# Performance work log

Measured on AMD Instinct MI355X. Metric: run time of the kernel, lower is better.

The kernel has to match this reference:

```python
import jax, jax.numpy as jnp
import numpy as np

B, T, D = 1, 2048, 2048
H, HD = 16, 128          # n_heads, head_dim
RD = 64                  # rotary_emb_dim
K = 4                    # short conv kernel size
EPS = 1e-5


def setup_inputs() -> dict:
    key = jax.random.key(0)
    ks = jax.random.split(key, 10)
    hidden_states = jax.random.normal(ks[0], (B, T, D), dtype=jnp.float32)
    # standard RoPE tables for the rotary sub-dimension
    inv_freq = 1.0 / (10000.0 ** (jnp.arange(0, RD, 2, dtype=jnp.float32) / RD))  # [RD/2]
    pos = jnp.arange(T, dtype=jnp.float32)
    freqs = pos[:, None] * inv_freq[None, :]          # [T, RD/2]
    emb = jnp.concatenate([freqs, freqs], axis=-1)    # [T, RD]
    cos = jnp.broadcast_to(jnp.cos(emb)[None], (B, T, RD))
    sin = jnp.broadcast_to(jnp.sin(emb)[None], (B, T, RD))
    s = 1.0 / np.sqrt(D)
    return {
        "hidden_states": hidden_states,
        "cos": cos, "sin": sin,
        "Wq": jax.random.normal(ks[1], (D, D), jnp.float32) * s,
        "Wk": jax.random.normal(ks[2], (D, D), jnp.float32) * s,
        "Wv": jax.random.normal(ks[3], (D, D), jnp.float32) * s,
        "Wo": jax.random.normal(ks[4], (D, D), jnp.float32) * s,
        "conv_q_w": jax.random.normal(ks[5], (D, K), jnp.float32) * 0.5,
        "conv_k_w": jax.random.normal(ks[6], (D, K), jnp.float32) * 0.5,
        "conv_v_w": jax.random.normal(ks[7], (D, K), jnp.float32) * 0.5,
        "q_norm_w": jnp.ones((HD,), jnp.float32),
        "k_norm_w": jnp.ones((HD,), jnp.float32),
    }


def _causal_conv_silu(x, w):
    # x: [B,T,D], w: [D,K]; depthwise causal conv (tap K-1 hits current pos) + SiLU
    xp = jnp.pad(x, ((0, 0), (K - 1, 0), (0, 0)))
    y = sum(xp[:, j:j + T, :] * w[None, None, :, j] for j in range(K))
    return jax.nn.silu(y)


def _rms_norm(x, w):
    # x: [..., HD]
    var = jnp.mean(x * x, axis=-1, keepdims=True)
    return x * jax.lax.rsqrt(var + EPS) * w


def _rotate_half(x):
    x1, x2 = x[..., : x.shape[-1] // 2], x[..., x.shape[-1] // 2:]
    return jnp.concatenate([-x2, x1], axis=-1)


def _apply_rope(x, cos, sin):
    # x: [B,H,T,HD]; cos/sin: [B,T,RD] -> unsqueeze head dim; partial rotary branch
    cos = cos[:, None, :, :]
    sin = sin[:, None, :, :]
    x_rot, x_pass = x[..., :RD], x[..., RD:]
    x_rot = x_rot * cos + _rotate_half(x_rot) * sin
    # faithful to source: negates rotated part when rotary_dim != head_dim
    return jnp.concatenate([-x_rot, x_pass], axis=-1)


def reference(hidden_states, cos, sin, Wq, Wk, Wv, Wo,
              conv_q_w, conv_k_w, conv_v_w, q_norm_w, k_norm_w):
    # projections (Linear with bias=False: y = x @ W^T)
    q = hidden_states @ Wq.T
    k = hidden_states @ Wk.T
    v = hidden_states @ Wv.T
    # short causal depthwise conv + SiLU
    q = _causal_conv_silu(q, conv_q_w)
    k = _causal_conv_silu(k, conv_k_w)
    v = _causal_conv_silu(v, conv_v_w)
    # split heads: [B,T,D] -> [B,T,H,HD]
    q = q.reshape(B, T, H, HD)
    k = k.reshape(B, T, H, HD)
    v = v.reshape(B, T, H, HD)
    # per-head RMSNorm, then [B,H,T,HD]
    q = _rms_norm(q, q_norm_w).transpose(0, 2, 1, 3)
    k = _rms_norm(k, k_norm_w).transpose(0, 2, 1, 3)
    v = v.transpose(0, 2, 1, 3)
    # RoPE (partial)
    q = _apply_rope(q, cos, sin)
    k = _apply_rope(k, cos, sin)
    # causal attention
    scale = 1.0 / np.sqrt(HD)
    scores = jnp.einsum('bhqd,bhkd->bhqk', q, k) * scale
    causal = jnp.tril(jnp.ones((T, T), dtype=bool))
    scores = jnp.where(causal[None, None], scores, jnp.float32(-1e30))
    probs = jax.nn.softmax(scores, axis=-1)
    attn = jnp.einsum('bhqk,bhkd->bhqd', probs, v)
    # [B,H,T,HD] -> [B,T,D], output projection
    out = attn.transpose(0, 2, 1, 3).reshape(B, T, D) @ Wo.T
    return out
```

## Files before the change

kernel.cpp:

```cpp
#include <hip/hip_runtime.h>
#include <hip/hip_bf16.h>

#define T_SEQ 2048
#define D_MODEL 2048
#define NH 16
#define HDIM 128
#define RD_ROT 64

typedef __bf16 bf16x8 __attribute__((ext_vector_type(8)));
typedef float f32x4 __attribute__((ext_vector_type(4)));

__device__ __forceinline__ void async_copy16(const __bf16* g, __bf16* l) {
    __builtin_amdgcn_global_load_lds(
        (const __attribute__((address_space(1))) void*)g,
        (__attribute__((address_space(3))) void*)l, 16, 0, 0);
}

__global__ __launch_bounds__(256) void cast_kernel(
    const float* __restrict__ s0, const float* __restrict__ s1, const float* __restrict__ s2,
    const float* __restrict__ s3, const float* __restrict__ s4,
    __bf16* __restrict__ d0, __bf16* __restrict__ d1, __bf16* __restrict__ d2,
    __bf16* __restrict__ d3, __bf16* __restrict__ d4)
{
    const float* s; __bf16* d;
    switch (blockIdx.y) {
        case 0: s = s0; d = d0; break;
        case 1: s = s1; d = d1; break;
        case 2: s = s2; d = d2; break;
        case 3: s = s3; d = d3; break;
        default: s = s4; d = d4; break;
    }
    size_t base = (size_t)blockIdx.x * D_MODEL + (size_t)threadIdx.x * 8;
    f32x4 a = *(const f32x4*)(s + base);
    f32x4 b = *(const f32x4*)(s + base + 4);
    bf16x8 o;
    #pragma unroll
    for (int i = 0; i < 4; i++) { o[i] = (__bf16)a[i]; o[i + 4] = (__bf16)b[i]; }
    *(bf16x8*)(d + base) = o;
}

__global__ __launch_bounds__(256) void gemm_bt_kernel(
    const __bf16* __restrict__ A,
    const __bf16* __restrict__ B0, const __bf16* __restrict__ B1, const __bf16* __restrict__ B2,
    __bf16* __restrict__ C0, __bf16* __restrict__ C1, __bf16* __restrict__ C2)
{
    constexpr int BM = 128, BK = 64, KD = D_MODEL;
    const __bf16* Bm = blockIdx.z == 0 ? B0 : (blockIdx.z == 1 ? B1 : B2);
    __bf16* Cm       = blockIdx.z == 0 ? C0 : (blockIdx.z == 1 ? C1 : C2);

    __shared__ __align__(16) __bf16 As[BM * BK];
    __shared__ __align__(16) __bf16 Bs[BM * BK];

    const int lane = threadIdx.x & 63;
    const int wave = threadIdx.x >> 6;
    const int r15  = lane & 15;
    const int quad = lane >> 4;
    const int bm = blockIdx.x * BM;
    const int bn = blockIdx.y * BM;
    const int wm = (wave >> 1) * 64;
    const int wn = (wave & 1) * 64;

    f32x4 acc[4][4] = {};

    const int srow_l = lane >> 3;
    const int sg     = lane & 7;

    for (int k0 = 0; k0 < KD; k0 += BK) {
        #pragma unroll
        for (int c = 0; c < 4; c++) {
            int row = wave * 32 + c * 8 + srow_l;
            int g = sg ^ (row & 7);
            async_copy16(A  + (size_t)(bm + row) * KD + k0 + g * 8, &As[(wave * 32 + c * 8) * BK]);
            async_copy16(Bm + (size_t)(bn + row) * KD + k0 + g * 8, &Bs[(wave * 32 + c * 8) * BK]);
        }
        __syncthreads();

        #pragma unroll
        for (int kc = 0; kc < 2; kc++) {
            bf16x8 av[4], bv[4];
            #pragma unroll
            for (int mt = 0; mt < 4; mt++)
                av[mt] = *(const bf16x8*)&As[(wm + mt * 16 + r15) * BK + (((kc * 4 + quad) ^ (r15 & 7)) << 3)];
            #pragma unroll
            for (int nt = 0; nt < 4; nt++)
                bv[nt] = *(const bf16x8*)&Bs[(wn + nt * 16 + r15) * BK + (((kc * 4 + quad) ^ (r15 & 7)) << 3)];
            #pragma unroll
            for (int mt = 0; mt < 4; mt++)
                #pragma unroll
                for (int nt = 0; nt < 4; nt++)
                    acc[mt][nt] = __builtin_amdgcn_mfma_f32_16x16x32_bf16(av[mt], bv[nt], acc[mt][nt], 0, 0, 0);
        }
        __syncthreads();
    }

    #pragma unroll
    for (int mt = 0; mt < 4; mt++) {
        #pragma unroll
        for (int r = 0; r < 4; r++) {
            size_t row = bm + wm + mt * 16 + quad * 4 + r;
            #pragma unroll
            for (int nt = 0; nt < 4; nt++) {
                size_t col = bn + wn + nt * 16 + r15;
                Cm[row * D_MODEL + col] = (__bf16)acc[mt][nt][r];
            }
        }
    }
}

__global__ __launch_bounds__(256) void gemm_bt_splitk_kernel(
    const __bf16* __restrict__ A, const __bf16* __restrict__ Bm, float* __restrict__ C)
{
    constexpr int BM = 128, BK = 64, KD = D_MODEL;
    __shared__ __align__(16) __bf16 As[BM * BK];
    __shared__ __align__(16) __bf16 Bs[BM * BK];

    const int lane = threadIdx.x & 63;
    const int wave = threadIdx.x >> 6;
    const int r15  = lane & 15;
    const int quad = lane >> 4;
    const int bm = blockIdx.x * BM;
    const int bn = blockIdx.y * BM;
    const int wm = (wave >> 1) * 64;
    const int wn = (wave & 1) * 64;
    const int kbase = blockIdx.z * (KD / 2);

    f32x4 acc[4][4] = {};
    const int srow_l = lane >> 3;
    const int sg     = lane & 7;

    for (int k0 = kbase; k0 < kbase + KD / 2; k0 += BK) {
        #pragma unroll
        for (int c = 0; c < 4; c++) {
            int row = wave * 32 + c * 8 + srow_l;
            int g = sg ^ (row & 7);
            async_copy16(A  + (size_t)(bm + row) * KD + k0 + g * 8, &As[(wave * 32 + c * 8) * BK]);
            async_copy16(Bm + (size_t)(bn + row) * KD + k0 + g * 8, &Bs[(wave * 32 + c * 8) * BK]);
        }
        __syncthreads();

        #pragma unroll
        for (int kc = 0; kc < 2; kc++) {
            bf16x8 av[4], bv[4];
            #pragma unroll
            for (int mt = 0; mt < 4; mt++)
                av[mt] = *(const bf16x8*)&As[(wm + mt * 16 + r15) * BK + (((kc * 4 + quad) ^ (r15 & 7)) << 3)];
            #pragma unroll
            for (int nt = 0; nt < 4; nt++)
                bv[nt] = *(const bf16x8*)&Bs[(wn + nt * 16 + r15) * BK + (((kc * 4 + quad) ^ (r15 & 7)) << 3)];
            #pragma unroll
            for (int mt = 0; mt < 4; mt++)
                #pragma unroll
                for (int nt = 0; nt < 4; nt++)
                    acc[mt][nt] = __builtin_amdgcn_mfma_f32_16x16x32_bf16(av[mt], bv[nt], acc[mt][nt], 0, 0, 0);
        }
        __syncthreads();
    }

    #pragma unroll
    for (int mt = 0; mt < 4; mt++) {
        #pragma unroll
        for (int r = 0; r < 4; r++) {
            size_t row = bm + wm + mt * 16 + quad * 4 + r;
            #pragma unroll
            for (int nt = 0; nt < 4; nt++) {
                size_t col = bn + wn + nt * 16 + r15;
                atomicAdd(&C[row * D_MODEL + col], acc[mt][nt][r]);
            }
        }
    }
}

__global__ __launch_bounds__(256) void preproc_qk_kernel(
    const __bf16* __restrict__ q_raw, const __bf16* __restrict__ k_raw,
    const float* __restrict__ cwq, const float* __restrict__ cwk,
    const float* __restrict__ qnw, const float* __restrict__ knw,
    const float* __restrict__ cosb, const float* __restrict__ sinb,
    __bf16* __restrict__ q_proc, __bf16* __restrict__ k_proc)
{
    const int t = blockIdx.x;
    const int which = blockIdx.y;
    const __bf16* X = which ? k_raw : q_raw;
    const float*  W = which ? cwk : cwq;
    const float*  nw = which ? knw : qnw;
    __bf16* P = which ? k_proc : q_proc;
    const float SC = which ? 1.0f : 0.08838834764831845f;

    const int tid = threadIdx.x;
    const int c0  = tid * 8;
    const int h   = tid >> 4;
    const int dl0 = (tid & 15) * 8;

    f32x4 wv[8];
    #pragma unroll
    for (int i = 0; i < 8; i++) wv[i] = *(const f32x4*)&W[(c0 + i) * 4];

    float acc[8] = {};
    #pragma unroll
    for (int j = 0; j < 4; j++) {
        int tt = t + j - 3;
        if (tt >= 0) {
            bf16x8 xv = *(const bf16x8*)&X[(size_t)tt * D_MODEL + c0];
            #pragma unroll
            for (int i = 0; i < 8; i++) acc[i] += (float)xv[i] * wv[i][j];
        }
    }
    float sil[8], ss = 0.f;
    #pragma unroll
    for (int i = 0; i < 8; i++) {
        float s = acc[i] / (1.f + __expf(-acc[i]));
        sil[i] = s; ss += s * s;
    }
    #pragma unroll
    for (int off = 1; off < 16; off <<= 1) ss += __shfl_xor(ss, off);
    float inv = rsqrtf(ss * (1.f / 128.f) + 1e-5f);

    f32x4 nv0 = *(const f32x4*)&nw[dl0];
    f32x4 nv1 = *(const f32x4*)&nw[dl0 + 4];
    float yn[8];
    #pragma unroll
    for (int i = 0; i < 8; i++) yn[i] = sil[i] * inv * (i < 4 ? nv0[i] : nv1[i - 4]);

    float partner[8];
    #pragma unroll
    for (int i = 0; i < 8; i++) partner[i] = __shfl_xor(yn[i], 4);

    bf16x8 o;
    if (dl0 < RD_ROT) {
        f32x4 cv0 = *(const f32x4*)&cosb[t * RD_ROT + dl0];
        f32x4 cv1 = *(const f32x4*)&cosb[t * RD_ROT + dl0 + 4];
        f32x4 sv0 = *(const f32x4*)&sinb[t * RD_ROT + dl0];
        f32x4 sv1 = *(const f32x4*)&sinb[t * RD_ROT + dl0 + 4];
        #pragma unroll
        for (int i = 0; i < 8; i++) {
            int dl = dl0 + i;
            float c = i < 4 ? cv0[i] : cv1[i - 4];
            float s = i < 4 ? sv0[i] : sv1[i - 4];
            float rot = (dl < 32) ? -partner[i] : partner[i];
            o[i] = (__bf16)((yn[i] * c + rot * s) * SC);
        }
    } else {
        #pragma unroll
        for (int i = 0; i < 8; i++) o[i] = (__bf16)(yn[i] * SC);
    }
    *(bf16x8*)&P[((size_t)h * T_SEQ + t) * HDIM + dl0] = o;
}

__global__ __launch_bounds__(128) void preproc_v_kernel(
    const __bf16* __restrict__ v_raw, const float* __restrict__ cwv,
    __bf16* __restrict__ v_t)
{
    const int t0 = blockIdx.x * 8;
    const int h = blockIdx.y;
    const int dl = threadIdx.x;
    const int d = h * HDIM + dl;

    f32x4 wv = *(const f32x4*)&cwv[d * 4];
    float x[11];
    #pragma unroll
    for (int m = 0; m < 11; m++) {
        int tt = t0 - 3 + m;
        x[m] = (tt >= 0) ? (float)v_raw[(size_t)tt * D_MODEL + d] : 0.f;
    }
    bf16x8 o;
    #pragma unroll
    for (int r = 0; r < 8; r++) {
        float y = x[r] * wv[0] + x[r + 1] * wv[1] + x[r + 2] * wv[2] + x[r + 3] * wv[3];
        o[r] = (__bf16)(y / (1.f + __expf(-y)));
    }
    *(bf16x8*)&v_t[((size_t)h * HDIM + dl) * T_SEQ + t0] = o;
}

__global__ __launch_bounds__(256, 2) void attn_kernel(
    const __bf16* __restrict__ Qp,
    const __bf16* __restrict__ Kp,
    const __bf16* __restrict__ Vt,
    __bf16* __restrict__ Op)
{
    constexpr int TK = 64, PSTR = 72;
    __shared__ __align__(16) __bf16 Ks[2][TK * HDIM];
    __shared__ __align__(16) __bf16 Vs[2][HDIM * TK];
    __shared__ __align__(16) __bf16 Ps[64 * PSTR];

    const int lane = threadIdx.x & 63;
    const int wave = threadIdx.x >> 6;
    const int r15  = lane & 15;
    const int quad = lane >> 4;
    const int h = blockIdx.y;
    const int qi = (blockIdx.y & 8) ? ((int)gridDim.x - 1 - (int)blockIdx.x) : (int)blockIdx.x;
    const int q0 = qi * TK;

    const __bf16* Kb = Kp + (size_t)h * T_SEQ * HDIM;
    const __bf16* Vb = Vt + (size_t)h * HDIM * T_SEQ;

    const int kchunk = wave * 4;
    const int krow_l = (lane >> 4);
    const int kg     = lane & 15;
    const int vrow_l = (lane >> 3);
    const int vg     = lane & 7;

    bf16x8 qf[4];
    const __bf16* qbase = Qp + ((size_t)h * T_SEQ + q0 + wave * 16 + r15) * HDIM;
    #pragma unroll
    for (int s = 0; s < 4; s++) qf[s] = *(const bf16x8*)(qbase + s * 32 + quad * 8);

    f32x4 oacc[8] = {};
    float lsum[4] = {};

    const int ntk = qi + 1;

    #pragma unroll
    for (int i = 0; i < 4; i++) {
        int ck = kchunk + i;
        int krow = ck * 4 + krow_l;
        int vrow = ck * 8 + vrow_l;
        async_copy16(Kb + (size_t)krow * HDIM + (kg ^ (krow & 15)) * 8, &Ks[0][ck * 512]);
        async_copy16(Vb + (size_t)vrow * T_SEQ + (vg ^ (vrow & 7)) * 8, &Vs[0][ck * 512]);
    }

    for (int it = 0; it < ntk; it++) {
        const int buf = it & 1;
        const bool last = (it == ntk - 1);
        __syncthreads();

        if (!last) {
            const int tkn = (it + 1) * TK;
            const int nbuf = buf ^ 1;
            #pragma unroll
            for (int i = 0; i < 4; i++) {
                int ck = kchunk + i;
                int krow = ck * 4 + krow_l;
                int vrow = ck * 8 + vrow_l;
                async_copy16(Kb + (size_t)(tkn + krow) * HDIM + (kg ^ (krow & 15)) * 8, &Ks[nbuf][ck * 512]);
                async_copy16(Vb + (size_t)vrow * T_SEQ + tkn + (vg ^ (vrow & 7)) * 8, &Vs[nbuf][ck * 512]);
            }
        }

        f32x4 sacc[4] = {};
        #pragma unroll
        for (int s = 0; s < 4; s++) {
            #pragma unroll
            for (int nt = 0; nt < 4; nt++) {
                bf16x8 kf = *(const bf16x8*)&Ks[buf][(nt * 16 + r15) * HDIM + (((s * 4 + quad) ^ r15) << 3)];
                sacc[nt] = __builtin_amdgcn_mfma_f32_16x16x32_bf16(qf[s], kf, sacc[nt], 0, 0, 0);
            }
        }

        #pragma unroll
        for (int nt = 0; nt < 4; nt++) {
            #pragma unroll
            for (int r = 0; r < 4; r++) {
                float p = __expf(sacc[nt][r]);
                if (last) {
                    int qrow = q0 + wave * 16 + quad * 4 + r;
                    int kcol = it * TK + nt * 16 + r15;
                    if (kcol > qrow) p = 0.f;
                }
                sacc[nt][r] = p;
                lsum[r] += p;
            }
        }

        #pragma unroll
        for (int nt = 0; nt < 4; nt++)
            #pragma unroll
            for (int r = 0; r < 4; r++)
                Ps[(wave * 16 + quad * 4 + r) * PSTR + nt * 16 + r15] = (__bf16)sacc[nt][r];

        #pragma unroll
        for (int s2 = 0; s2 < 2; s2++) {
            bf16x8 pf = *(const bf16x8*)&Ps[(wave * 16 + r15) * PSTR + s2 * 32 + quad * 8];
            #pragma unroll
            for (int nt = 0; nt < 8; nt++) {
                bf16x8 vf = *(const bf16x8*)&Vs[buf][(nt * 16 + r15) * TK + (((s2 * 4 + quad) ^ (r15 & 7)) << 3)];
                oacc[nt] = __builtin_amdgcn_mfma_f32_16x16x32_bf16(pf, vf, oacc[nt], 0, 0, 0);
            }
        }
    }

    #pragma unroll
    for (int r = 0; r < 4; r++) {
        float l = lsum[r];
        #pragma unroll
        for (int off = 1; off < 16; off <<= 1) l += __shfl_xor(l, off);
        float inv = 1.0f / l;
        size_t row = q0 + wave * 16 + quad * 4 + r;
        #pragma unroll
        for (int nt = 0; nt < 8; nt++)
            Op[row * D_MODEL + h * HDIM + nt * 16 + r15] = (__bf16)(oacc[nt][r] * inv);
    }
}

extern "C" void kernel_launch(void* const* d_in, const int* in_sizes, int n_in,
                              void* d_out, int out_size, void* d_ws, size_t ws_size,
                              hipStream_t stream) {
    (void)in_sizes; (void)n_in; (void)out_size; (void)ws_size;
    const float* hidden = (const float*)d_in[0];
    const float* cosb   = (const float*)d_in[1];
    const float* sinb   = (const float*)d_in[2];
    const float* Wq     = (const float*)d_in[3];
    const float* Wk     = (const float*)d_in[4];
    const float* Wv     = (const float*)d_in[5];
    const float* Wo     = (const float*)d_in[6];
    const float* cwq    = (const float*)d_in[7];
    const float* cwk    = (const float*)d_in[8];
    const float* cwv    = (const float*)d_in[9];
    const float* qnw    = (const float*)d_in[10];
    const float* knw    = (const float*)d_in[11];

    const size_t NEL = (size_t)T_SEQ * D_MODEL;
    __bf16* ws = (__bf16*)d_ws;
    __bf16* h_bf   = ws + 0 * NEL;
    __bf16* Wq_bf  = ws + 1 * NEL;
    __bf16* Wk_bf  = ws + 2 * NEL;
    __bf16* Wv_bf  = ws + 3 * NEL;
    __bf16* Wo_bf  = ws + 4 * NEL;
    __bf16* q_raw  = ws + 5 * NEL;
    __bf16* k_raw  = ws + 6 * NEL;
    __bf16* v_raw  = ws + 7 * NEL;
    __bf16* q_proc = Wq_bf;
    __bf16* k_proc = Wk_bf;
    __bf16* v_t    = Wv_bf;
    __bf16* attn_b = h_bf;
    float*  out    = (float*)d_out;

    cast_kernel<<<dim3(T_SEQ, 5), 256, 0, stream>>>(hidden, Wq, Wk, Wv, Wo,
                                                    h_bf, Wq_bf, Wk_bf, Wv_bf, Wo_bf);
    gemm_bt_kernel<<<dim3(16, 16, 3), 256, 0, stream>>>(
        h_bf, Wq_bf, Wk_bf, Wv_bf, q_raw, k_raw, v_raw);
    preproc_qk_kernel<<<dim3(T_SEQ, 2), 256, 0, stream>>>(
        q_raw, k_raw, cwq, cwk, qnw, knw, cosb, sinb, q_proc, k_proc);
    preproc_v_kernel<<<dim3(T_SEQ / 8, NH), 128, 0, stream>>>(v_raw, cwv, v_t);
    attn_kernel<<<dim3(T_SEQ / 64, NH), 256, 0, stream>>>(q_proc, k_proc, v_t, attn_b);
    hipMemsetAsync(d_out, 0, NEL * sizeof(float), stream);
    gemm_bt_splitk_kernel<<<dim3(16, 16, 2), 256, 0, stream>>>(attn_b, Wo_bf, out);
}
```

Baseline: 346.1 us.

## Double-buffer GEMM LDS tiles with BK=32 to overlap loads and MFMA

Both projection GEMM kernels switch from a single LDS buffer with BK=64 to two ping-pong buffers with BK=32. The global-to-LDS async copy for the next K slice is issued right after the barrier, so it can run while the MFMAs work on the current slice, and one barrier per iteration is removed. The XOR swizzle is adjusted to the 4-chunk row width. The cost is twice as many loop iterations and barriers, with less MFMA work per barrier.

```diff
diff --git a/kernel.cpp b/kernel.cpp
--- a/kernel.cpp
+++ b/kernel.cpp
@@ -44,12 +44,12 @@
     const __bf16* __restrict__ B0, const __bf16* __restrict__ B1, const __bf16* __restrict__ B2,
     __bf16* __restrict__ C0, __bf16* __restrict__ C1, __bf16* __restrict__ C2)
 {
-    constexpr int BM = 128, BK = 64, KD = D_MODEL;
+    constexpr int BM = 128, BK = 32, KD = D_MODEL, NIT = KD / BK;
     const __bf16* Bm = blockIdx.z == 0 ? B0 : (blockIdx.z == 1 ? B1 : B2);
     __bf16* Cm       = blockIdx.z == 0 ? C0 : (blockIdx.z == 1 ? C1 : C2);
 
-    __shared__ __align__(16) __bf16 As[BM * BK];
-    __shared__ __align__(16) __bf16 Bs[BM * BK];
+    __shared__ __align__(16) __bf16 As[2][BM * BK];
+    __shared__ __align__(16) __bf16 Bs[2][BM * BK];
 
     const int lane = threadIdx.x & 63;
     const int wave = threadIdx.x >> 6;
@@ -62,35 +62,44 @@
 
     f32x4 acc[4][4] = {};
 
-    const int srow_l = lane >> 3;
-    const int sg     = lane & 7;
-
-    for (int k0 = 0; k0 < KD; k0 += BK) {
-        #pragma unroll
-        for (int c = 0; c < 4; c++) {
-            int row = wave * 32 + c * 8 + srow_l;
-            int g = sg ^ (row & 7);
-            async_copy16(A  + (size_t)(bm + row) * KD + k0 + g * 8, &As[(wave * 32 + c * 8) * BK]);
-            async_copy16(Bm + (size_t)(bn + row) * KD + k0 + g * 8, &Bs[(wave * 32 + c * 8) * BK]);
-        }
+    const int srow = wave * 32 + (lane >> 2);
+    const int sg   = (lane & 3) ^ ((lane >> 2) & 3);
+
+    const __bf16* Arow0 = A  + (size_t)(bm + srow)      * KD + sg * 8;
+    const __bf16* Arow1 = A  + (size_t)(bm + srow + 16) * KD + sg * 8;
+    const __bf16* Brow0 = Bm + (size_t)(bn + srow)      * KD + sg * 8;
+    const __bf16* Brow1 = Bm + (size_t)(bn + srow + 16) * KD + sg * 8;
+
+    async_copy16(Arow0, &As[0][wave * 1024]);
+    async_copy16(Arow1, &As[0][wave * 1024 + 512]);
+    async_copy16(Brow0, &Bs[0][wave * 1024]);
+    async_copy16(Brow1, &Bs[0][wave * 1024 + 512]);
+
+    for (int it = 0; it < NIT; it++) {
+        const int buf = it & 1;
         __syncthreads();
 
-        #pragma unroll
-        for (int kc = 0; kc < 2; kc++) {
-            bf16x8 av[4], bv[4];
-            #pragma unroll
-            for (int mt = 0; mt < 4; mt++)
-                av[mt] = *(const bf16x8*)&As[(wm + mt * 16 + r15) * BK + (((kc * 4 + quad) ^ (r15 & 7)) << 3)];
+        if (it + 1 < NIT) {
+            const int k0 = (it + 1) * BK;
+            const int nb = buf ^ 1;
+            async_copy16(Arow0 + k0, &As[nb][wave * 1024]);
+            async_copy16(Arow1 + k0, &As[nb][wave * 1024 + 512]);
+            async_copy16(Brow0 + k0, &Bs[nb][wave * 1024]);
+            async_copy16(Brow1 + k0, &Bs[nb][wave * 1024 + 512]);
+        }
+
+        bf16x8 av[4], bv[4];
+        #pragma unroll
+        for (int mt = 0; mt < 4; mt++)
+            av[mt] = *(const bf16x8*)&As[buf][(wm + mt * 16 + r15) * BK + ((quad ^ (r15 & 3)) << 3)];
+        #pragma unroll
+        for (int nt = 0; nt < 4; nt++)
+            bv[nt] = *(const bf16x8*)&Bs[buf][(wn + nt * 16 + r15) * BK + ((quad ^ (r15 & 3)) << 3)];
+        #pragma unroll
+        for (int mt = 0; mt < 4; mt++)
             #pragma unroll
             for (int nt = 0; nt < 4; nt++)
-                bv[nt] = *(const bf16x8*)&Bs[(wn + nt * 16 + r15) * BK + (((kc * 4 + quad) ^ (r15 & 7)) << 3)];
-            #pragma unroll
-            for (int mt = 0; mt < 4; mt++)
-                #pragma unroll
-                for (int nt = 0; nt < 4; nt++)
-                    acc[mt][nt] = __builtin_amdgcn_mfma_f32_16x16x32_bf16(av[mt], bv[nt], acc[mt][nt], 0, 0, 0);
-        }
-        __syncthreads();
+                acc[mt][nt] = __builtin_amdgcn_mfma_f32_16x16x32_bf16(av[mt], bv[nt], acc[mt][nt], 0, 0, 0);
     }
 
     #pragma unroll
@@ -110,9 +119,9 @@
 __global__ __launch_bounds__(256) void gemm_bt_splitk_kernel(
     const __bf16* __restrict__ A, const __bf16* __restrict__ Bm, float* __restrict__ C)
 {
-    constexpr int BM = 128, BK = 64, KD = D_MODEL;
-    __shared__ __align__(16) __bf16 As[BM * BK];
-    __shared__ __align__(16) __bf16 Bs[BM * BK];
+    constexpr int BM = 128, BK = 32, KD = D_MODEL, NIT = (KD / 2) / BK;
+    __shared__ __align__(16) __bf16 As[2][BM * BK];
+    __shared__ __align__(16) __bf16 Bs[2][BM * BK];
 
     const int lane = threadIdx.x & 63;
     const int wave = threadIdx.x >> 6;
@@ -125,35 +134,44 @@
     const int kbase = blockIdx.z * (KD / 2);
 
     f32x4 acc[4][4] = {};
-    const int srow_l = lane >> 3;
-    const int sg     = lane & 7;
-
-    for (int k0 = kbase; k0 < kbase + KD / 2; k0 += BK) {
-        #pragma unroll
-        for (int c = 0; c < 4; c++) {
-            int row = wave * 32 + c * 8 + srow_l;
-            int g = sg ^ (row & 7);
-            async_copy16(A  + (size_t)(bm + row) * KD + k0 + g * 8, &As[(wave * 32 + c * 8) * BK]);
-            async_copy16(Bm + (size_t)(bn + row) * KD + k0 + g * 8, &Bs[(wave * 32 + c * 8) * BK]);
-        }
+    const int srow = wave * 32 + (lane >> 2);
+    const int sg   = (lane & 3) ^ ((lane >> 2) & 3);
+
+    const __bf16* Arow0 = A  + (size_t)(bm + srow)      * KD + kbase + sg * 8;
+    const __bf16* Arow1 = A  + (size_t)(bm + srow + 16) * KD + kbase + sg * 8;
+    const __bf16* Brow0 = Bm + (size_t)(bn + srow)      * KD + kbase + sg * 8;
+    const __bf16* Brow1 = Bm + (size_t)(bn + srow + 16) * KD + kbase + sg * 8;
+
+    async_copy16(Arow0, &As[0][wave * 1024]);
+    async_copy16(Arow1, &As[0][wave * 1024 + 512]);
+    async_copy16(Brow0, &Bs[0][wave * 1024]);
+    async_copy16(Brow1, &Bs[0][wave * 1024 + 512]);
+
+    for (int it = 0; it < NIT; it++) {
+        const int buf = it & 1;
         __syncthreads();
 
-        #pragma unroll
-        for (int kc = 0; kc < 2; kc++) {
-            bf16x8 av[4], bv[4];
-            #pragma unroll
-            for (int mt = 0; mt < 4; mt++)
-                av[mt] = *(const bf16x8*)&As[(wm + mt * 16 + r15) * BK + (((kc * 4 + quad) ^ (r15 & 7)) << 3)];
+        if (it + 1 < NIT) {
+            const int k0 = (it + 1) * BK;
+            const int nb = buf ^ 1;
+            async_copy16(Arow0 + k0, &As[nb][wave * 1024]);
+            async_copy16(Arow1 + k0, &As[nb][wave * 1024 + 512]);
+            async_copy16(Brow0 + k0, &Bs[nb][wave * 1024]);
+            async_copy16(Brow1 + k0, &Bs[nb][wave * 1024 + 512]);
+        }
+
+        bf16x8 av[4], bv[4];
+        #pragma unroll
+        for (int mt = 0; mt < 4; mt++)
+            av[mt] = *(const bf16x8*)&As[buf][(wm + mt * 16 + r15) * BK + ((quad ^ (r15 & 3)) << 3)];
+        #pragma unroll
+        for (int nt = 0; nt < 4; nt++)
+            bv[nt] = *(const bf16x8*)&Bs[buf][(wn + nt * 16 + r15) * BK + ((quad ^ (r15 & 3)) << 3)];
+        #pragma unroll
+        for (int mt = 0; mt < 4; mt++)
             #pragma unroll
             for (int nt = 0; nt < 4; nt++)
-                bv[nt] = *(const bf16x8*)&Bs[(wn + nt * 16 + r15) * BK + (((kc * 4 + quad) ^ (r15 & 7)) << 3)];
-            #pragma unroll
-            for (int mt = 0; mt < 4; mt++)
-                #pragma unroll
-                for (int nt = 0; nt < 4; nt++)
-                    acc[mt][nt] = __builtin_amdgcn_mfma_f32_16x16x32_bf16(av[mt], bv[nt], acc[mt][nt], 0, 0, 0);
-        }
-        __syncthreads();
+                acc[mt][nt] = __builtin_amdgcn_mfma_f32_16x16x32_bf16(av[mt], bv[nt], acc[mt][nt], 0, 0, 0);
     }
 
     #pragma unroll
```

Result: no change. 341.6 us (-1.3%).
